# Optimization experiments

Hardware: AMD Instinct MI355X
Metric: run time of the kernel (lower is better)

## Reference

```python
import jax, jax.numpy as jnp
import numpy as np

B, C, H, W = 4, 256, 128, 128
HEADS, KD, VD = 8, 64, 64
EPS = 1e-5


def setup_inputs() -> dict:
    key = jax.random.key(0)
    ks = jax.random.split(key, 5)
    s = 0.02
    return {
        "x": jax.random.normal(ks[0], (B, C, H, W), dtype=jnp.float32),
        "wq": jax.random.normal(ks[1], (HEADS * KD, C), dtype=jnp.float32) * s,
        "bq": jnp.zeros((HEADS * KD,), dtype=jnp.float32),
        "wk": jax.random.normal(ks[2], (HEADS * KD, C), dtype=jnp.float32) * s,
        "bk": jnp.zeros((HEADS * KD,), dtype=jnp.float32),
        "wv": jax.random.normal(ks[3], (HEADS * VD, C), dtype=jnp.float32) * s,
        "bv": jnp.zeros((HEADS * VD,), dtype=jnp.float32),
        "wo": jax.random.normal(ks[4], (C, HEADS * VD), dtype=jnp.float32) * s,
        "bo": jnp.zeros((C,), dtype=jnp.float32),
        "g_q": jnp.ones((KD,), dtype=jnp.float32),
        "be_q": jnp.zeros((KD,), dtype=jnp.float32),
        "g_k": jnp.ones((KD,), dtype=jnp.float32),
        "be_k": jnp.zeros((KD,), dtype=jnp.float32),
        "g_v": jnp.ones((VD,), dtype=jnp.float32),
        "be_v": jnp.zeros((VD,), dtype=jnp.float32),
    }


def _conv1x1(t, w, b):
    # t: [B,C,H,W], w: [O,C] -> [B,O,H,W]
    return jnp.einsum("bchw,oc->bohw", t, w) + b[None, :, None, None]


def _ln_dim(t, g, be):
    # LayerNorm over the per-head feature axis (axis=2) of [B,heads,dim,N]
    mu = jnp.mean(t, axis=2, keepdims=True)
    var = jnp.var(t, axis=2, keepdims=True)
    return (t - mu) * jax.lax.rsqrt(var + EPS) * g[None, None, :, None] + be[None, None, :, None]


def reference(x, wq, bq, wk, bk, wv, bv, wo, bo, g_q, be_q, g_k, be_k, g_v, be_v):
    b, c, h, w = x.shape
    n = h * w
    # context defaults to x
    q = _conv1x1(x, wq, bq).reshape(b, HEADS, KD, n)
    k = _conv1x1(x, wk, bk).reshape(b, HEADS, KD, n)
    v = _conv1x1(x, wv, bv).reshape(b, HEADS, VD, n)
    q = _ln_dim(q, g_q, be_q)
    k = _ln_dim(k, g_k, be_k)
    v = _ln_dim(v, g_v, be_v)
    q = jax.nn.softmax(q * (KD ** -0.25), axis=2)  # softmax over key_dim
    k = jax.nn.softmax(k, axis=3)                  # softmax over N
    ctx = jnp.einsum("bhkn,bhvn->bhkv", k, v)      # [B,heads,KD,VD]
    out = jnp.einsum("bhkn,bhkv->bhvn", q, ctx)    # [B,heads,VD,N]
    out = out.reshape(b, HEADS * VD, h, w)
    return _conv1x1(out, wo, bo)
```

## Files before the change

### kernel.cpp

```cpp
#include <hip/hip_runtime.h>
#include <hip/hip_bf16.h>
#include <stdint.h>

typedef unsigned short u16;
typedef __attribute__((__vector_size__(16))) short s16x8;
typedef __attribute__((__vector_size__(16))) float f32x4;

#define N_ 16384
#define C_ 256

__device__ __forceinline__ float bf2f(u16 u) {
    union { uint32_t i; float f; } v; v.i = ((uint32_t)u) << 16; return v.f;
}
__device__ __forceinline__ u16 f2bf(float f) {
    union { uint32_t i; float f; } v; v.f = f;
    uint32_t u = v.i;
    return (u16)((u + 0x7FFFu + ((u >> 16) & 1u)) >> 16);
}

__device__ __forceinline__ void gl_lds16(const u16* g, u16* l) {
    __builtin_amdgcn_global_load_lds((__attribute__((address_space(1))) void*)g,
                                     (__attribute__((address_space(3))) void*)l,
                                     16, 0, 0);
}

__global__ __launch_bounds__(256) void zero_kernel(float* __restrict__ p, int n) {
    int i = blockIdx.x * 256 + threadIdx.x;
    if (i < n) p[i] = 0.f;
}

__global__ __launch_bounds__(256) void transpose_kernel(const float* __restrict__ x,
                                                        u16* __restrict__ xT) {
    __shared__ float T[64][65];
    int tid = threadIdx.x;
    int n0 = blockIdx.x * 64, c0 = blockIdx.y * 64, b = blockIdx.z;
    const float* xp = x + (size_t)b * C_ * N_;
    for (int it = 0; it < 16; it++) {
        int idx = it * 256 + tid;
        int c = idx >> 6, n = idx & 63;
        T[c][n] = xp[(size_t)(c0 + c) * N_ + n0 + n];
    }
    __syncthreads();
    u16* op = xT + (size_t)b * N_ * C_;
    for (int it = 0; it < 8; it++) {
        int idx = it * 256 + tid;
        int n = idx >> 5, c2 = (idx & 31) * 2;
        uint32_t lo = f2bf(T[c2][n]);
        uint32_t hi = f2bf(T[c2 + 1][n]);
        *(uint32_t*)&op[(size_t)(n0 + n) * C_ + c0 + c2] = lo | (hi << 16);
    }
}

__global__ __launch_bounds__(256) void cvtw_kernel(const float* __restrict__ wq,
                                                   const float* __restrict__ wk,
                                                   const float* __restrict__ wv,
                                                   u16* __restrict__ wb) {
    int m = blockIdx.y;
    const float* s = m == 0 ? wq : (m == 1 ? wk : wv);
    int i = blockIdx.x * 256 + threadIdx.x;
    wb[(size_t)m * 131072 + i] = f2bf(s[i]);
}


#define STAGE2(WSRC, XSRC, LDW, KC, CUR) {                                         \
    int koff_ = (KC) * 64 + sc8;                                                   \
    _Pragma("unroll")                                                              \
    for (int i_ = 0; i_ < 4; i_++) {                                               \
        int row_ = (wid * 4 + i_) * 8 + srow;                                      \
        gl_lds16(&(WSRC)[(size_t)row_ * (LDW) + koff_], &SH[CUR][(wid * 4 + i_) * 512]);      \
        gl_lds16(&(XSRC)[(size_t)row_ * (LDW) + koff_], &SH[2 + (CUR)][(wid * 4 + i_) * 512]); \
    } }

__global__ __launch_bounds__(256) void kv_kernel(
    const u16* __restrict__ xT, const u16* __restrict__ wb,
    const float* __restrict__ bk, const float* __restrict__ bv,
    const float* __restrict__ gk, const float* __restrict__ bek,
    const float* __restrict__ gv, const float* __restrict__ bev,
    u16* __restrict__ eKb, u16* __restrict__ vbb, float* __restrict__ rs)
{
    __shared__ u16 SH[4][8192];
    int tid = threadIdx.x;
    int lane = tid & 63, wid = tid >> 6;
    int quad = lane >> 4, l15 = lane & 15;
    int wm = wid >> 1, wn = wid & 1;
    int bx = blockIdx.x, sec = blockIdx.y, b = blockIdx.z;
    int kind2 = sec >> 2, pair = sec & 3;
    int r0 = pair * 128;
    int n0 = bx * 128;

    const float* bptr  = kind2 ? bv  : bk;
    const float* gptr  = kind2 ? gv  : gk;
    const float* beptr = kind2 ? bev : bek;
    const u16* wsrc = wb + (size_t)(1 + kind2) * 131072 + (size_t)r0 * 256;
    const u16* xsrc = xT + ((size_t)b * N_ + n0) * 256;

    f32x4 acc[4][4];
#pragma unroll
    for (int i = 0; i < 4; i++)
#pragma unroll
        for (int j = 0; j < 4; j++) acc[i][j] = (f32x4){0.f, 0.f, 0.f, 0.f};

    int srow = lane >> 3;
    int sc8  = ((lane & 7) ^ srow) * 8;

    STAGE2(wsrc, xsrc, 256, 0, 0);
    __syncthreads();
    for (int kc = 0; kc < 4; kc++) {
        int cur = kc & 1;
        if (kc < 3) STAGE2(wsrc, xsrc, 256, kc + 1, cur ^ 1);
        const u16* Wb = &SH[cur][0];
        const u16* Xb = &SH[2 + cur][0];
#pragma unroll
        for (int ks = 0; ks < 2; ks++) {
            int cc = ks * 4 + quad;
            s16x8 af[4], bf[4];
#pragma unroll
            for (int f = 0; f < 4; f++) {
                int ar = wn * 64 + f * 16 + l15;
                int br = wm * 64 + f * 16 + l15;
                af[f] = *(const s16x8*)&Xb[ar * 64 + ((cc ^ (ar & 7)) * 8)];
                bf[f] = *(const s16x8*)&Wb[br * 64 + ((cc ^ (br & 7)) * 8)];
            }
#pragma unroll
            for (int i = 0; i < 4; i++)
#pragma unroll
                for (int j = 0; j < 4; j++)
                    acc[i][j] = __builtin_amdgcn_mfma_f32_16x16x32_bf16(af[i], bf[j], acc[i][j], 0, 0, 0);
        }
        if (kc < 3) __syncthreads();
    }

    int head = pair * 2 + wm;
    float bB_[4], gB[4], eB[4];
#pragma unroll
    for (int nf = 0; nf < 4; nf++) {
        int rl = nf * 16 + l15;
        bB_[nf] = bptr[head * 64 + rl];
        gB[nf]  = gptr[rl];
        eB[nf]  = beptr[rl];
    }
#pragma unroll
    for (int mf = 0; mf < 4; mf++)
#pragma unroll
        for (int nf = 0; nf < 4; nf++)
#pragma unroll
            for (int r = 0; r < 4; r++) acc[mf][nf][r] += bB_[nf];
    float sa[4][4], sb[4][4];
#pragma unroll
    for (int mf = 0; mf < 4; mf++)
#pragma unroll
        for (int r = 0; r < 4; r++) {
            float s = 0.f, s2 = 0.f;
#pragma unroll
            for (int nf = 0; nf < 4; nf++) { float v = acc[mf][nf][r]; s += v; s2 += v * v; }
            sa[mf][r] = s; sb[mf][r] = s2;
        }
#pragma unroll
    for (int msk = 1; msk <= 8; msk <<= 1)
#pragma unroll
        for (int mf = 0; mf < 4; mf++)
#pragma unroll
            for (int r = 0; r < 4; r++) {
                sa[mf][r] += __shfl_xor(sa[mf][r], msk);
                sb[mf][r] += __shfl_xor(sb[mf][r], msk);
            }
#pragma unroll
    for (int mf = 0; mf < 4; mf++)
#pragma unroll
        for (int r = 0; r < 4; r++) {
            float mu = sa[mf][r] * (1.f / 64.f);
            float rstd = rsqrtf(sb[mf][r] * (1.f / 64.f) - mu * mu + 1e-5f);
#pragma unroll
            for (int nf = 0; nf < 4; nf++)
                acc[mf][nf][r] = (acc[mf][nf][r] - mu) * rstd * gB[nf] + eB[nf];
        }
    if (kind2 == 0) {
#pragma unroll
        for (int mf = 0; mf < 4; mf++)
#pragma unroll
            for (int nf = 0; nf < 4; nf++)
#pragma unroll
                for (int r = 0; r < 4; r++) acc[mf][nf][r] = __expf(acc[mf][nf][r]);
#pragma unroll
        for (int nf = 0; nf < 4; nf++) {
            float s = 0.f;
#pragma unroll
            for (int mf = 0; mf < 4; mf++)
#pragma unroll
                for (int r = 0; r < 4; r++) s += acc[mf][nf][r];
            s += __shfl_xor(s, 16); s += __shfl_xor(s, 32);
            if (quad == 0)
                atomicAdd(&rs[(size_t)b * 512 + head * 64 + nf * 16 + l15], s);
        }
    }
    u16* op = (kind2 == 0) ? eKb : vbb;
    u16* st = (wm == 0) ? &SH[0][0] : &SH[2][0];
#pragma unroll
    for (int mf = 0; mf < 4; mf++)
#pragma unroll
        for (int nf = 0; nf < 4; nf++) {
            int rh = nf * 16 + l15;
            int ln = wn * 64 + mf * 16 + quad * 4;
            int c  = ln >> 3;
            int off = rh * 128 + ((c ^ (rh & 15)) * 8) + (ln & 7);
            uint64_t w0 = (uint64_t)f2bf(acc[mf][nf][0]) | ((uint64_t)f2bf(acc[mf][nf][1]) << 16) |
                          ((uint64_t)f2bf(acc[mf][nf][2]) << 32) | ((uint64_t)f2bf(acc[mf][nf][3]) << 48);
            *(uint64_t*)&st[off] = w0;
        }
    __syncthreads();
    {
        int tile = tid >> 7, t = tid & 127;
        const u16* src = (tile == 0) ? &SH[0][0] : &SH[2][0];
        int headt = pair * 2 + tile;
        size_t tb = ((size_t)((b * 8 + headt) * 128 + bx)) * 8192;
#pragma unroll
        for (int i = 0; i < 8; i++) {
            int j = (i * 128 + t) * 8;
            *(s16x8*)&op[tb + j] = *(const s16x8*)&src[j];
        }
    }
}

__global__ __launch_bounds__(256) void q_kernel(
    const u16* __restrict__ xT, const u16* __restrict__ wb,
    const float* __restrict__ bq, const float* __restrict__ gq, const float* __restrict__ beq,
    u16* __restrict__ qT)
{
    __shared__ u16 SH[4][8192];
    int tid = threadIdx.x;
    int lane = tid & 63, wid = tid >> 6;
    int quad = lane >> 4, l15 = lane & 15;
    int wm = wid >> 1, wn = wid & 1;
    int bx = blockIdx.x, pair = blockIdx.y, b = blockIdx.z;
    int r0 = pair * 128;
    int n0 = bx * 128;

    const u16* wsrc = wb + (size_t)r0 * 256;
    const u16* xsrc = xT + ((size_t)b * N_ + n0) * 256;

    f32x4 acc[4][4];
#pragma unroll
    for (int i = 0; i < 4; i++)
#pragma unroll
        for (int j = 0; j < 4; j++) acc[i][j] = (f32x4){0.f, 0.f, 0.f, 0.f};

    int srow = lane >> 3;
    int sc8  = ((lane & 7) ^ srow) * 8;

    STAGE2(wsrc, xsrc, 256, 0, 0);
    __syncthreads();
    for (int kc = 0; kc < 4; kc++) {
        int cur = kc & 1;
        if (kc < 3) STAGE2(wsrc, xsrc, 256, kc + 1, cur ^ 1);
        const u16* Wb = &SH[cur][0];
        const u16* Xb = &SH[2 + cur][0];
#pragma unroll
        for (int ks = 0; ks < 2; ks++) {
            int cc = ks * 4 + quad;
            s16x8 af[4], bf[4];
#pragma unroll
            for (int f = 0; f < 4; f++) {
                int ar = wm * 64 + f * 16 + l15;
                int br = wn * 64 + f * 16 + l15;
                af[f] = *(const s16x8*)&Wb[ar * 64 + ((cc ^ (ar & 7)) * 8)];
                bf[f] = *(const s16x8*)&Xb[br * 64 + ((cc ^ (br & 7)) * 8)];
            }
#pragma unroll
            for (int i = 0; i < 4; i++)
#pragma unroll
                for (int j = 0; j < 4; j++)
                    acc[i][j] = __builtin_amdgcn_mfma_f32_16x16x32_bf16(af[i], bf[j], acc[i][j], 0, 0, 0);
        }
        if (kc < 3) __syncthreads();
    }

    float bA[4][4], gA[4][4], eA[4][4];
#pragma unroll
    for (int mf = 0; mf < 4; mf++)
#pragma unroll
        for (int r = 0; r < 4; r++) {
            int rl = mf * 16 + quad * 4 + r;
            bA[mf][r] = bq[r0 + wm * 64 + rl];
            gA[mf][r] = gq[rl];
            eA[mf][r] = beq[rl];
        }
#pragma unroll
    for (int mf = 0; mf < 4; mf++)
#pragma unroll
        for (int nf = 0; nf < 4; nf++)
#pragma unroll
            for (int r = 0; r < 4; r++) acc[mf][nf][r] += bA[mf][r];
#pragma unroll
    for (int nf = 0; nf < 4; nf++) {
        float s = 0.f, s2 = 0.f;
#pragma unroll
        for (int mf = 0; mf < 4; mf++)
#pragma unroll
            for (int r = 0; r < 4; r++) { float v = acc[mf][nf][r]; s += v; s2 += v * v; }
        s  += __shfl_xor(s, 16);  s  += __shfl_xor(s, 32);
        s2 += __shfl_xor(s2, 16); s2 += __shfl_xor(s2, 32);
        float mu = s * (1.f / 64.f);
        float rstd = rsqrtf(s2 * (1.f / 64.f) - mu * mu + 1e-5f);
#pragma unroll
        for (int mf = 0; mf < 4; mf++)
#pragma unroll
            for (int r = 0; r < 4; r++)
                acc[mf][nf][r] = (acc[mf][nf][r] - mu) * rstd * gA[mf][r] + eA[mf][r];
    }
    const float s_q = 0.35355339059327373f;
#pragma unroll
    for (int nf = 0; nf < 4; nf++) {
        float m = -1e30f;
#pragma unroll
        for (int mf = 0; mf < 4; mf++)
#pragma unroll
            for (int r = 0; r < 4; r++) { acc[mf][nf][r] *= s_q; m = fmaxf(m, acc[mf][nf][r]); }
        m = fmaxf(m, __shfl_xor(m, 16)); m = fmaxf(m, __shfl_xor(m, 32));
        float d = 0.f;
#pragma unroll
        for (int mf = 0; mf < 4; mf++)
#pragma unroll
            for (int r = 0; r < 4; r++) { float e = __expf(acc[mf][nf][r] - m); acc[mf][nf][r] = e; d += e; }
        d += __shfl_xor(d, 16); d += __shfl_xor(d, 32);
        float inv = 1.f / d;
#pragma unroll
        for (int mf = 0; mf < 4; mf++)
#pragma unroll
            for (int r = 0; r < 4; r++) acc[mf][nf][r] *= inv;
    }
    u16* st = (wn == 0) ? &SH[0][0] : &SH[2][0];
#pragma unroll
    for (int mf = 0; mf < 4; mf++)
#pragma unroll
        for (int nf = 0; nf < 4; nf++) {
            int nl = nf * 16 + l15;
            int gl = wm * 64 + mf * 16 + quad * 4;
            int c  = gl >> 3;
            int off = nl * 128 + ((c ^ (nl & 15)) * 8) + (gl & 7);
            uint64_t w0 = (uint64_t)f2bf(acc[mf][nf][0]) | ((uint64_t)f2bf(acc[mf][nf][1]) << 16) |
                          ((uint64_t)f2bf(acc[mf][nf][2]) << 32) | ((uint64_t)f2bf(acc[mf][nf][3]) << 48);
            *(uint64_t*)&st[off] = w0;
        }
    __syncthreads();
    {
        u16* qp = qT + (size_t)b * N_ * 512;
#pragma unroll
        for (int i = 0; i < 8; i++) {
            int idx = i * 256 + tid;
            int n = idx >> 4, cp = idx & 15;
            const u16* src = (n < 64) ? &SH[0][0] : &SH[2][0];
            int nl = n & 63;
            s16x8 v = *(const s16x8*)&src[nl * 128 + ((cp ^ (nl & 15)) * 8)];
            *(s16x8*)&qp[(size_t)(n0 + n) * 512 + r0 + cp * 8] = v;
        }
    }
}

__global__ __launch_bounds__(256) void ctx_kernel(
    const u16* __restrict__ eKb, const u16* __restrict__ vbb,
    float* __restrict__ ctx_acc)
{
    __shared__ u16 ES[64 * 128];
    __shared__ u16 VS[64 * 128];
    __shared__ float CTXS[64 * 66];
    int tid = threadIdx.x;
    int lane = tid & 63, wid = tid >> 6;
    int quad = lane >> 4, l15 = lane & 15;
    int ns = blockIdx.x, h = blockIdx.y, b = blockIdx.z;
    for (int i = tid; i < 64 * 66; i += 256) CTXS[i] = 0.f;
    size_t hb = (size_t)(b * 8 + h) * 128;
    f32x4 acc[4][4];
#pragma unroll
    for (int i = 0; i < 4; i++)
#pragma unroll
        for (int j = 0; j < 4; j++) acc[i][j] = (f32x4){0.f, 0.f, 0.f, 0.f};

    for (int t = 0; t < 8; t++) {
        size_t tb = (hb + ns * 8 + t) * 8192;
#pragma unroll
        for (int i = 0; i < 4; i++) {
            size_t g = tb + ((size_t)((wid * 4 + i) * 64) + lane) * 8;
            gl_lds16(&eKb[g], &ES[(wid * 4 + i) * 512]);
            gl_lds16(&vbb[g], &VS[(wid * 4 + i) * 512]);
        }
        __syncthreads();
        int cc = wid * 4 + quad;
        s16x8 af[4], bf[4];
#pragma unroll
        for (int f = 0; f < 4; f++) {
            int off = (f * 16 + l15) * 128 + ((cc ^ l15) * 8);
            af[f] = *(const s16x8*)&ES[off];
            bf[f] = *(const s16x8*)&VS[off];
        }
#pragma unroll
        for (int i = 0; i < 4; i++)
#pragma unroll
            for (int j = 0; j < 4; j++)
                acc[i][j] = __builtin_amdgcn_mfma_f32_16x16x32_bf16(af[i], bf[j], acc[i][j], 0, 0, 0);
        __syncthreads();
    }
#pragma unroll
    for (int mf = 0; mf < 4; mf++)
#pragma unroll
        for (int nf = 0; nf < 4; nf++)
#pragma unroll
            for (int r = 0; r < 4; r++) {
                int kd = mf * 16 + quad * 4 + r, vd = nf * 16 + l15;
                atomicAdd(&CTXS[kd * 66 + vd], acc[mf][nf][r]);
            }
    __syncthreads();
    size_t base = ((size_t)b * 8 + h) * 4096;
    for (int i = tid; i < 4096; i += 256)
        atomicAdd(&ctx_acc[base + i], CTXS[(i >> 6) * 66 + (i & 63)]);
}

__global__ __launch_bounds__(256) void weff_kernel(
    const float* __restrict__ ctx_acc, const float* __restrict__ rs,
    const float* __restrict__ wo, u16* __restrict__ Weffb)
{
    __shared__ float CT[16][65];
    int tid = threadIdx.x;
    int h = blockIdx.x, b = blockIdx.y, kc = blockIdx.z;
    for (int i = tid; i < 1024; i += 256) {
        int kdl = i >> 6, vd = i & 63;
        int kd = kc * 16 + kdl;
        CT[kdl][vd] = ctx_acc[(((size_t)b * 8 + h) * 64 + kd) * 64 + vd] /
                      rs[(size_t)b * 512 + h * 64 + kd];
    }
    __syncthreads();
    int c = tid;
    float wrow[64];
    const float4* wp = (const float4*)(wo + (size_t)c * 512 + h * 64);
#pragma unroll
    for (int i = 0; i < 16; i++) { float4 t = wp[i]; wrow[i*4] = t.x; wrow[i*4+1] = t.y; wrow[i*4+2] = t.z; wrow[i*4+3] = t.w; }
    for (int kdl = 0; kdl < 16; kdl++) {
        float s = 0.f;
#pragma unroll
        for (int vd = 0; vd < 64; vd++) s += wrow[vd] * CT[kdl][vd];
        Weffb[((size_t)b * 256 + c) * 512 + h * 64 + kc * 16 + kdl] = f2bf(s);
    }
}

__global__ __launch_bounds__(256) void out_kernel(
    const u16* __restrict__ Weffb, const u16* __restrict__ qT,
    const float* __restrict__ bo, float* __restrict__ out)
{
    __shared__ u16 SH[4][8192];
    int tid = threadIdx.x;
    int lane = tid & 63, wid = tid >> 6;
    int quad = lane >> 4, l15 = lane & 15;
    int wm = wid >> 1, wn = wid & 1;
    int n0 = blockIdx.x * 128, c0 = blockIdx.y * 128, b = blockIdx.z;
    const u16* asrc = Weffb + ((size_t)b * 256 + c0) * 512;
    const u16* bsrc = qT + ((size_t)b * N_ + n0) * 512;

    f32x4 acc[4][4];
#pragma unroll
    for (int i = 0; i < 4; i++)
#pragma unroll
        for (int j = 0; j < 4; j++) acc[i][j] = (f32x4){0.f, 0.f, 0.f, 0.f};

    int srow = lane >> 3;
    int sc8  = ((lane & 7) ^ srow) * 8;

    STAGE2(asrc, bsrc, 512, 0, 0);
    __syncthreads();
    for (int kc = 0; kc < 8; kc++) {
        int cur = kc & 1;
        if (kc < 7) STAGE2(asrc, bsrc, 512, kc + 1, cur ^ 1);
        const u16* Wb = &SH[cur][0];
        const u16* Xb = &SH[2 + cur][0];
#pragma unroll
        for (int ks = 0; ks < 2; ks++) {
            int cc = ks * 4 + quad;
            s16x8 af[4], bf[4];
#pragma unroll
            for (int f = 0; f < 4; f++) {
                int ar = wm * 64 + f * 16 + l15;
                int br = wn * 64 + f * 16 + l15;
                af[f] = *(const s16x8*)&Wb[ar * 64 + ((cc ^ (ar & 7)) * 8)];
                bf[f] = *(const s16x8*)&Xb[br * 64 + ((cc ^ (br & 7)) * 8)];
            }
#pragma unroll
            for (int i = 0; i < 4; i++)
#pragma unroll
                for (int j = 0; j < 4; j++)
                    acc[i][j] = __builtin_amdgcn_mfma_f32_16x16x32_bf16(af[i], bf[j], acc[i][j], 0, 0, 0);
        }
        if (kc < 7) __syncthreads();
    }
#pragma unroll
    for (int mf = 0; mf < 4; mf++)
#pragma unroll
        for (int r = 0; r < 4; r++) {
            int c = c0 + wm * 64 + mf * 16 + quad * 4 + r;
            float bov = bo[c];
#pragma unroll
            for (int nf = 0; nf < 4; nf++)
                out[((size_t)b * 256 + c) * N_ + n0 + wn * 64 + nf * 16 + l15] = acc[mf][nf][r] + bov;
        }
}

extern "C" void kernel_launch(void* const* d_in, const int* in_sizes, int n_in,
                              void* d_out, int out_size, void* d_ws, size_t ws_size,
                              hipStream_t stream) {
    const float* x   = (const float*)d_in[0];
    const float* wq  = (const float*)d_in[1];
    const float* bq  = (const float*)d_in[2];
    const float* wk  = (const float*)d_in[3];
    const float* bk  = (const float*)d_in[4];
    const float* wv  = (const float*)d_in[5];
    const float* bv  = (const float*)d_in[6];
    const float* wo  = (const float*)d_in[7];
    const float* bo  = (const float*)d_in[8];
    const float* gq  = (const float*)d_in[9];
    const float* beq = (const float*)d_in[10];
    const float* gk  = (const float*)d_in[11];
    const float* bek = (const float*)d_in[12];
    const float* gv  = (const float*)d_in[13];
    const float* bev = (const float*)d_in[14];
    float* out = (float*)d_out;

    char* ws = (char*)d_ws;
    u16* xT      = (u16*)(ws);
    u16* wb      = (u16*)(ws + 33554432ULL);
    u16* eKb     = (u16*)(ws + 34340864ULL);
    u16* qT      = (u16*)(ws + 34340864ULL);
    u16* vbb     = (u16*)(ws + 101449728ULL);
    float* ctx_a = (float*)(ws + 168558592ULL);
    float* rs    = (float*)(ws + 169082880ULL);
    u16* Weffb   = (u16*)(ws + 169091072ULL);

    cvtw_kernel<<<dim3(512, 3), 256, 0, stream>>>(wq, wk, wv, wb);
    transpose_kernel<<<dim3(256, 4, 4), 256, 0, stream>>>(x, xT);
    zero_kernel<<<dim3(520), 256, 0, stream>>>(ctx_a, 133120);

    kv_kernel<<<dim3(128, 8, 4), 256, 0, stream>>>(
        xT, wb, bk, bv, gk, bek, gv, bev, eKb, vbb, rs);

    ctx_kernel<<<dim3(16, 8, 4), 256, 0, stream>>>(eKb, vbb, ctx_a);

    q_kernel<<<dim3(128, 4, 4), 256, 0, stream>>>(xT, wb, bq, gq, beq, qT);

    weff_kernel<<<dim3(8, 4, 4), 256, 0, stream>>>(ctx_a, rs, wo, Weffb);

    out_kernel<<<dim3(128, 2, 4), 256, 0, stream>>>(Weffb, qT, bo, out);
}
```

Before: 380.3 us.

## Fuse K/V projection with context GEMM, dropping intermediate eK/V buffers

The K and V projection kernel is restructured so that each block computes both K and V for one head over a 128-pixel tile. It then immediately multiplies exp(K) by V in LDS to form a partial context matrix, which replaces the separate ctx_kernel. The change removes the round trip of bf16 eK and V through global memory (about 128MB written and read) and one kernel launch. In exchange it adds a large number of global float atomics into 8 striped context slices, which weff now sums. It also adds zeroing of an 8x larger context buffer and of rs.

```diff
diff --git a/kernel.cpp b/kernel.cpp
--- a/kernel.cpp
+++ b/kernel.cpp
@@ -71,27 +71,23 @@
         gl_lds16(&(XSRC)[(size_t)row_ * (LDW) + koff_], &SH[2 + (CUR)][(wid * 4 + i_) * 512]); \
     } }
 
-__global__ __launch_bounds__(256) void kv_kernel(
+__global__ __launch_bounds__(256) void kvctx_kernel(
     const u16* __restrict__ xT, const u16* __restrict__ wb,
     const float* __restrict__ bk, const float* __restrict__ bv,
     const float* __restrict__ gk, const float* __restrict__ bek,
     const float* __restrict__ gv, const float* __restrict__ bev,
-    u16* __restrict__ eKb, u16* __restrict__ vbb, float* __restrict__ rs)
+    float* __restrict__ ctx8, float* __restrict__ rs)
 {
-    __shared__ u16 SH[4][8192];
+    __shared__ u16 SH[4][8704];
     int tid = threadIdx.x;
     int lane = tid & 63, wid = tid >> 6;
     int quad = lane >> 4, l15 = lane & 15;
     int wm = wid >> 1, wn = wid & 1;
-    int bx = blockIdx.x, sec = blockIdx.y, b = blockIdx.z;
-    int kind2 = sec >> 2, pair = sec & 3;
-    int r0 = pair * 128;
+    int bx = blockIdx.x, h = blockIdx.y, b = blockIdx.z;
     int n0 = bx * 128;
 
-    const float* bptr  = kind2 ? bv  : bk;
-    const float* gptr  = kind2 ? gv  : gk;
-    const float* beptr = kind2 ? bev : bek;
-    const u16* wsrc = wb + (size_t)(1 + kind2) * 131072 + (size_t)r0 * 256;
+    const u16* wsrcw = wb + (size_t)(1 + (wid >> 1)) * 131072
+                          + ((size_t)h * 64 + (size_t)(wid & 1) * 32) * 256;
     const u16* xsrc = xT + ((size_t)b * N_ + n0) * 256;
 
     f32x4 acc[4][4];
@@ -103,11 +99,20 @@
     int srow = lane >> 3;
     int sc8  = ((lane & 7) ^ srow) * 8;
 
-    STAGE2(wsrc, xsrc, 256, 0, 0);
+#define STAGEF(KC, CUR) {                                                          \
+    int koff_ = (KC) * 64 + sc8;                                                   \
+    _Pragma("unroll")                                                              \
+    for (int i_ = 0; i_ < 4; i_++) {                                               \
+        int ri_ = i_ * 8 + srow;                                                   \
+        gl_lds16(&wsrcw[(size_t)ri_ * 256 + koff_], &SH[CUR][(wid * 4 + i_) * 512]); \
+        gl_lds16(&xsrc[(size_t)(wid * 32 + ri_) * 256 + koff_], &SH[2 + (CUR)][(wid * 4 + i_) * 512]); \
+    } }
+
+    STAGEF(0, 0);
     __syncthreads();
     for (int kc = 0; kc < 4; kc++) {
         int cur = kc & 1;
-        if (kc < 3) STAGE2(wsrc, xsrc, 256, kc + 1, cur ^ 1);
+        if (kc < 3) STAGEF(kc + 1, cur ^ 1);
         const u16* Wb = &SH[cur][0];
         const u16* Xb = &SH[2 + cur][0];
 #pragma unroll
@@ -130,12 +135,14 @@
         if (kc < 3) __syncthreads();
     }
 
-    int head = pair * 2 + wm;
+    const float* bptr  = wm ? bv  : bk;
+    const float* gptr  = wm ? gv  : gk;
+    const float* beptr = wm ? bev : bek;
     float bB_[4], gB[4], eB[4];
 #pragma unroll
     for (int nf = 0; nf < 4; nf++) {
         int rl = nf * 16 + l15;
-        bB_[nf] = bptr[head * 64 + rl];
+        bB_[nf] = bptr[h * 64 + rl];
         gB[nf]  = gptr[rl];
         eB[nf]  = beptr[rl];
     }
@@ -174,7 +181,7 @@
             for (int nf = 0; nf < 4; nf++)
                 acc[mf][nf][r] = (acc[mf][nf][r] - mu) * rstd * gB[nf] + eB[nf];
         }
-    if (kind2 == 0) {
+    if (wm == 0) {
 #pragma unroll
         for (int mf = 0; mf < 4; mf++)
 #pragma unroll
@@ -190,35 +197,80 @@
                 for (int r = 0; r < 4; r++) s += acc[mf][nf][r];
             s += __shfl_xor(s, 16); s += __shfl_xor(s, 32);
             if (quad == 0)
-                atomicAdd(&rs[(size_t)b * 512 + head * 64 + nf * 16 + l15], s);
-        }
-    }
-    u16* op = (kind2 == 0) ? eKb : vbb;
-    u16* st = (wm == 0) ? &SH[0][0] : &SH[2][0];
-#pragma unroll
-    for (int mf = 0; mf < 4; mf++)
-#pragma unroll
-        for (int nf = 0; nf < 4; nf++) {
-            int rh = nf * 16 + l15;
-            int ln = wn * 64 + mf * 16 + quad * 4;
-            int c  = ln >> 3;
-            int off = rh * 128 + ((c ^ (rh & 15)) * 8) + (ln & 7);
-            uint64_t w0 = (uint64_t)f2bf(acc[mf][nf][0]) | ((uint64_t)f2bf(acc[mf][nf][1]) << 16) |
-                          ((uint64_t)f2bf(acc[mf][nf][2]) << 32) | ((uint64_t)f2bf(acc[mf][nf][3]) << 48);
-            *(uint64_t*)&st[off] = w0;
-        }
-    __syncthreads();
+                atomicAdd(&rs[(size_t)b * 512 + h * 64 + nf * 16 + l15], s);
+        }
+    }
+
+    __syncthreads();
+    u16* ES = (u16*)SH;
+    u16* VS = ES + 8192;
     {
-        int tile = tid >> 7, t = tid & 127;
-        const u16* src = (tile == 0) ? &SH[0][0] : &SH[2][0];
-        int headt = pair * 2 + tile;
-        size_t tb = ((size_t)((b * 8 + headt) * 128 + bx)) * 8192;
-#pragma unroll
-        for (int i = 0; i < 8; i++) {
-            int j = (i * 128 + t) * 8;
-            *(s16x8*)&op[tb + j] = *(const s16x8*)&src[j];
-        }
-    }
+        u16* st = wm ? VS : ES;
+#pragma unroll
+        for (int mf = 0; mf < 4; mf++)
+#pragma unroll
+            for (int nf = 0; nf < 4; nf++) {
+                int rh = nf * 16 + l15;
+                int ln = wn * 64 + mf * 16 + quad * 4;
+                int c  = ln >> 3;
+                int off = rh * 128 + ((c ^ (rh & 15)) * 8) + (ln & 7);
+                uint64_t w0 = (uint64_t)f2bf(acc[mf][nf][0]) | ((uint64_t)f2bf(acc[mf][nf][1]) << 16) |
+                              ((uint64_t)f2bf(acc[mf][nf][2]) << 32) | ((uint64_t)f2bf(acc[mf][nf][3]) << 48);
+                *(uint64_t*)&st[off] = w0;
+            }
+    }
+    __syncthreads();
+    f32x4 cacc[4][4];
+#pragma unroll
+    for (int i = 0; i < 4; i++)
+#pragma unroll
+        for (int j = 0; j < 4; j++) cacc[i][j] = (f32x4){0.f, 0.f, 0.f, 0.f};
+    {
+        int cc = wid * 4 + quad;
+        s16x8 caf[4], cbf[4];
+#pragma unroll
+        for (int f = 0; f < 4; f++) {
+            int off = (f * 16 + l15) * 128 + ((cc ^ l15) * 8);
+            caf[f] = *(const s16x8*)&ES[off];
+            cbf[f] = *(const s16x8*)&VS[off];
+        }
+#pragma unroll
+        for (int i = 0; i < 4; i++)
+#pragma unroll
+            for (int j = 0; j < 4; j++)
+                cacc[i][j] = __builtin_amdgcn_mfma_f32_16x16x32_bf16(caf[i], cbf[j], cacc[i][j], 0, 0, 0);
+    }
+    __syncthreads();
+    {
+        float* CTXW = (float*)((char*)SH + (size_t)wid * 17408);
+#pragma unroll
+        for (int mf = 0; mf < 4; mf++)
+#pragma unroll
+            for (int nf = 0; nf < 4; nf++) {
+                int kd = mf * 16 + quad * 4, vd = nf * 16 + l15;
+                *(f32x4*)&CTXW[vd * 68 + kd] = cacc[mf][nf];
+            }
+    }
+    __syncthreads();
+    {
+        int vd = tid >> 2, kd0 = (tid & 3) * 16;
+        const float* C0 = (const float*)((char*)SH);
+        const float* C1 = (const float*)((char*)SH + 17408);
+        const float* C2 = (const float*)((char*)SH + 34816);
+        const float* C3 = (const float*)((char*)SH + 52224);
+        float* gctx = ctx8 + ((((size_t)(bx & 7) * 4 + b) * 8 + h) * 64 + vd) * 64 + kd0;
+#pragma unroll
+        for (int j4 = 0; j4 < 4; j4++) {
+            int o = vd * 68 + kd0 + j4 * 4;
+            f32x4 s = *(const f32x4*)&C0[o];
+            s += *(const f32x4*)&C1[o];
+            s += *(const f32x4*)&C2[o];
+            s += *(const f32x4*)&C3[o];
+#pragma unroll
+            for (int r = 0; r < 4; r++) atomicAdd(&gctx[j4 * 4 + r], s[r]);
+        }
+    }
+#undef STAGEF
 }
 
 __global__ __launch_bounds__(256) void q_kernel(
@@ -356,66 +408,8 @@
     }
 }
 
-__global__ __launch_bounds__(256) void ctx_kernel(
-    const u16* __restrict__ eKb, const u16* __restrict__ vbb,
-    float* __restrict__ ctx_acc)
-{
-    __shared__ u16 ES[64 * 128];
-    __shared__ u16 VS[64 * 128];
-    __shared__ float CTXS[64 * 66];
-    int tid = threadIdx.x;
-    int lane = tid & 63, wid = tid >> 6;
-    int quad = lane >> 4, l15 = lane & 15;
-    int ns = blockIdx.x, h = blockIdx.y, b = blockIdx.z;
-    for (int i = tid; i < 64 * 66; i += 256) CTXS[i] = 0.f;
-    size_t hb = (size_t)(b * 8 + h) * 128;
-    f32x4 acc[4][4];
-#pragma unroll
-    for (int i = 0; i < 4; i++)
-#pragma unroll
-        for (int j = 0; j < 4; j++) acc[i][j] = (f32x4){0.f, 0.f, 0.f, 0.f};
-
-    for (int t = 0; t < 8; t++) {
-        size_t tb = (hb + ns * 8 + t) * 8192;
-#pragma unroll
-        for (int i = 0; i < 4; i++) {
-            size_t g = tb + ((size_t)((wid * 4 + i) * 64) + lane) * 8;
-            gl_lds16(&eKb[g], &ES[(wid * 4 + i) * 512]);
-            gl_lds16(&vbb[g], &VS[(wid * 4 + i) * 512]);
-        }
-        __syncthreads();
-        int cc = wid * 4 + quad;
-        s16x8 af[4], bf[4];
-#pragma unroll
-        for (int f = 0; f < 4; f++) {
-            int off = (f * 16 + l15) * 128 + ((cc ^ l15) * 8);
-            af[f] = *(const s16x8*)&ES[off];
-            bf[f] = *(const s16x8*)&VS[off];
-        }
-#pragma unroll
-        for (int i = 0; i < 4; i++)
-#pragma unroll
-            for (int j = 0; j < 4; j++)
-                acc[i][j] = __builtin_amdgcn_mfma_f32_16x16x32_bf16(af[i], bf[j], acc[i][j], 0, 0, 0);
-        __syncthreads();
-    }
-#pragma unroll
-    for (int mf = 0; mf < 4; mf++)
-#pragma unroll
-        for (int nf = 0; nf < 4; nf++)
-#pragma unroll
-            for (int r = 0; r < 4; r++) {
-                int kd = mf * 16 + quad * 4 + r, vd = nf * 16 + l15;
-                atomicAdd(&CTXS[kd * 66 + vd], acc[mf][nf][r]);
-            }
-    __syncthreads();
-    size_t base = ((size_t)b * 8 + h) * 4096;
-    for (int i = tid; i < 4096; i += 256)
-        atomicAdd(&ctx_acc[base + i], CTXS[(i >> 6) * 66 + (i & 63)]);
-}
-
 __global__ __launch_bounds__(256) void weff_kernel(
-    const float* __restrict__ ctx_acc, const float* __restrict__ rs,
+    const float* __restrict__ ctx8, const float* __restrict__ rs,
     const float* __restrict__ wo, u16* __restrict__ Weffb)
 {
     __shared__ float CT[16][65];
@@ -424,8 +418,11 @@
     for (int i = tid; i < 1024; i += 256) {
         int kdl = i >> 6, vd = i & 63;
         int kd = kc * 16 + kdl;
-        CT[kdl][vd] = ctx_acc[(((size_t)b * 8 + h) * 64 + kd) * 64 + vd] /
-                      rs[(size_t)b * 512 + h * 64 + kd];
+        float s = 0.f;
+#pragma unroll
+        for (int sl = 0; sl < 8; sl++)
+            s += ctx8[((((size_t)sl * 4 + b) * 8 + h) * 64 + vd) * 64 + kd];
+        CT[kdl][vd] = s / rs[(size_t)b * 512 + h * 64 + kd];
     }
     __syncthreads();
     int c = tid;
@@ -524,25 +521,22 @@
     char* ws = (char*)d_ws;
     u16* xT      = (u16*)(ws);
     u16* wb      = (u16*)(ws + 33554432ULL);
-    u16* eKb     = (u16*)(ws + 34340864ULL);
     u16* qT      = (u16*)(ws + 34340864ULL);
-    u16* vbb     = (u16*)(ws + 101449728ULL);
-    float* ctx_a = (float*)(ws + 168558592ULL);
+    float* ctx8  = (float*)(ws + 101449728ULL);
     float* rs    = (float*)(ws + 169082880ULL);
     u16* Weffb   = (u16*)(ws + 169091072ULL);
 
     cvtw_kernel<<<dim3(512, 3), 256, 0, stream>>>(wq, wk, wv, wb);
     transpose_kernel<<<dim3(256, 4, 4), 256, 0, stream>>>(x, xT);
-    zero_kernel<<<dim3(520), 256, 0, stream>>>(ctx_a, 133120);
-
-    kv_kernel<<<dim3(128, 8, 4), 256, 0, stream>>>(
-        xT, wb, bk, bv, gk, bek, gv, bev, eKb, vbb, rs);
-
-    ctx_kernel<<<dim3(16, 8, 4), 256, 0, stream>>>(eKb, vbb, ctx_a);
+    zero_kernel<<<dim3(4096), 256, 0, stream>>>(ctx8, 1048576);
+    zero_kernel<<<dim3(8), 256, 0, stream>>>(rs, 2048);
+
+    kvctx_kernel<<<dim3(128, 8, 4), 256, 0, stream>>>(
+        xT, wb, bk, bv, gk, bek, gv, bev, ctx8, rs);
 
     q_kernel<<<dim3(128, 4, 4), 256, 0, stream>>>(xT, wb, bq, gq, beq, qT);
 
-    weff_kernel<<<dim3(8, 4, 4), 256, 0, stream>>>(ctx_a, rs, wo, Weffb);
+    weff_kernel<<<dim3(8, 4, 4), 256, 0, stream>>>(ctx8, rs, wo, Weffb);
 
     out_kernel<<<dim3(128, 2, 4), 256, 0, stream>>>(Weffb, qT, bo, out);
 }
```

After: 1.051 ms. +176.2%, slower.
